# Performance work log

Measured on AMD Instinct MI355X. Metric: run time of the kernel, lower is better.

The kernel has to match this reference:

```python
import jax, jax.numpy as jnp
import numpy as np

N = 120000   # nodes
E = 1200000  # edges
F_IN = 14    # PascalVOC-SP node features
H = 64       # args.hidden
C = 21       # num_classes
EPS = 1e-5


def _glorot(k, shape):
    fan_in = shape[0]
    return jax.random.normal(k, shape, jnp.float32) / np.sqrt(fan_in).astype(np.float32)


def setup_inputs() -> dict:
    key = jax.random.key(0)
    ks = jax.random.split(key, 16)
    inp = {}
    inp['x1'] = jax.random.normal(ks[0], (N, F_IN), jnp.float32)
    inp['edge_index'] = jax.random.randint(ks[1], (2, E), 0, N)
    dims = [(F_IN, H), (H, H), (H, H), (H, H)]
    i = 2
    for l, (din, dout) in enumerate(dims, 1):
        inp[f'Wn{l}'] = _glorot(ks[i], (din, dout)); i += 1
        inp[f'Wr{l}'] = _glorot(ks[i], (din, dout)); i += 1
        inp[f'b{l}'] = jnp.zeros((dout,), jnp.float32)
    for l in (1, 2, 3):
        inp[f'g{l}'] = jnp.ones((H,), jnp.float32)
        inp[f'be{l}'] = jnp.zeros((H,), jnp.float32)
    inp['Wm0'] = _glorot(ks[10], (H, H))
    inp['gm0'] = jnp.ones((H,), jnp.float32)
    inp['bem0'] = jnp.zeros((H,), jnp.float32)
    inp['Wm1'] = _glorot(ks[11], (H, H))
    inp['gm1'] = jnp.ones((H,), jnp.float32)
    inp['bem1'] = jnp.zeros((H,), jnp.float32)
    inp['Wm2'] = _glorot(ks[12], (H, C))
    inp['bm2'] = jnp.zeros((C,), jnp.float32)
    return inp


def _bn(x, g, b):
    # BatchNorm1d forward with batch statistics (train-mode normalization, biased var)
    m = x.mean(axis=0)
    v = x.var(axis=0)
    return (x - m) * jax.lax.rsqrt(v + EPS) * g + b


def _sage(x, src, dst, Wn, Wr, b):
    # PyG SAGEConv (mean aggr): out = mean_neighbors @ Wn + b + x @ Wr
    s = jax.ops.segment_sum(x[src], dst, num_segments=N)        # [N, d]
    cnt = jax.ops.segment_sum(jnp.ones((src.shape[0],), x.dtype), dst, num_segments=N)
    mean = s / jnp.maximum(cnt, 1.0)[:, None]
    return mean @ Wn + b + x @ Wr


def _lrelu(z):
    return jnp.where(z > 0, z, 0.01 * z)


def reference(x1, edge_index, Wn1, Wr1, b1, Wn2, Wr2, b2, Wn3, Wr3, b3, Wn4, Wr4, b4,
              g1, be1, g2, be2, g3, be3, Wm0, gm0, bem0, Wm1, gm1, bem1, Wm2, bm2):
    src, dst = edge_index[0], edge_index[1]
    x = _bn(_lrelu(_sage(x1, src, dst, Wn1, Wr1, b1)), g1, be1)   # conv1 + bano1 (dropout off)
    x = _bn(_lrelu(_sage(x, src, dst, Wn2, Wr2, b2)), g2, be2)    # conv2 + bano2
    x = _bn(jax.nn.relu(_sage(x, src, dst, Wn3, Wr3, b3)), g3, be3)  # conv3 + bano3
    x = _sage(x, src, dst, Wn4, Wr4, b4)                          # conv4
    # mlpRep: Linear(no bias)->BN->ReLU x2, then Linear(bias), no final act
    x = jax.nn.relu(_bn(x @ Wm0, gm0, bem0))
    x = jax.nn.relu(_bn(x @ Wm1, gm1, bem1))
    return x @ Wm2 + bm2
```

## Files before the change

kernel.cpp:

```cpp
#include <hip/hip_runtime.h>

constexpr int NN = 120000;
constexpr int EE = 1200000;
constexpr float EPSV = 1e-5f;
constexpr int NCBLK   = (NN + 127) / 128;
constexpr int NMFMABLK = NN / 64;
constexpr int ASTRIDE = 32;
constexpr int NSLOT = 64;

constexpr int BNODES  = 128;
constexpr int NBUCK   = (NN + BNODES - 1) / BNODES;
constexpr int BSTRIDE = 1536;
constexpr int EPB3    = 8192;
constexpr int NB3     = (EE + EPB3 - 1) / EPB3;

typedef __attribute__((ext_vector_type(8))) short bf8v;
typedef __attribute__((ext_vector_type(4))) float f4v;

__device__ __forceinline__ float bf2f(unsigned short u){
  union { unsigned i; float f; } v; v.i = ((unsigned)u) << 16; return v.f;
}
__device__ __forceinline__ unsigned short f2bf(float f){
  union { float f; unsigned i; } v; v.f = f;
  unsigned u = v.i;
  return (unsigned short)((u + 0x7FFFu + ((u >> 16) & 1u)) >> 16);
}
__device__ __forceinline__ unsigned pack2(float a, float b){
  return (unsigned)f2bf(a) | ((unsigned)f2bf(b) << 16);
}
__device__ __forceinline__ float act_f(float z, int ACT){
  if (ACT == 1) return z > 0.0f ? z : 0.01f*z;
  if (ACT == 2) return fmaxf(z, 0.0f);
  return z;
}
__device__ __forceinline__ void acc8(uint4 u, float& a0, float& a1, float& a2, float& a3,
                                     float& a4, float& a5, float& a6, float& a7){
  a0 += bf2f((unsigned short)(u.x & 0xFFFF)); a1 += bf2f((unsigned short)(u.x >> 16));
  a2 += bf2f((unsigned short)(u.y & 0xFFFF)); a3 += bf2f((unsigned short)(u.y >> 16));
  a4 += bf2f((unsigned short)(u.z & 0xFFFF)); a5 += bf2f((unsigned short)(u.z >> 16));
  a6 += bf2f((unsigned short)(u.w & 0xFFFF)); a7 += bf2f((unsigned short)(u.w >> 16));
}

__global__ __launch_bounds__(512) void k_bucket(const int* __restrict__ src, const int* __restrict__ dst,
                                                int* __restrict__ cursor, unsigned* __restrict__ bucketed){
  __shared__ int hist[NBUCK];
  __shared__ int lstart[NBUCK];
  const int tid = threadIdx.x;
  const int e0  = blockIdx.x * EPB3;
  for (int i = tid; i < NBUCK; i += 512) hist[i] = 0;
  __syncthreads();

  const bool full = (e0 + EPB3 <= EE);
  if (full){
    #pragma unroll 4
    for (int k = 0; k < EPB3/512; k++){
      int d = dst[e0 + k*512 + tid];
      atomicAdd(&hist[d >> 7], 1);
    }
  } else {
    #pragma unroll 1
    for (int k = 0; k < EPB3/512; k++){
      int e = e0 + k*512 + tid;
      if (e < EE){
        int d = dst[e];
        atomicAdd(&hist[d >> 7], 1);
      }
    }
  }
  __syncthreads();
  for (int i = tid; i < NBUCK; i += 512){
    int h = hist[i];
    lstart[i] = (h > 0) ? atomicAdd(&cursor[i], h) : 0;
  }
  __syncthreads();
  for (int i = tid; i < NBUCK; i += 512) hist[i] = 0;
  __syncthreads();
  #pragma unroll 1
  for (int k = 0; k < EPB3/512; k++){
    int e = e0 + k*512 + tid;
    if (e < EE){
      int d = dst[e];
      int s = src[e];
      int b = d >> 7;
      int r = atomicAdd(&hist[b], 1);
      int idx = lstart[b] + r;
      if (idx < BSTRIDE)
        bucketed[(size_t)b*BSTRIDE + idx] = ((unsigned)s << 7) | (unsigned)(d & 127);
    }
  }
}

__global__ __launch_bounds__(256) void k_buildadj(const unsigned* __restrict__ bucketed,
                                                  const int* __restrict__ cursor,
                                                  int* __restrict__ cnt, int* __restrict__ adj,
                                                  float* __restrict__ invdeg){
  __shared__ alignas(16) int ladj[BNODES*ASTRIDE];
  __shared__ int lcnt[BNODES];
  const int tid = threadIdx.x;
  const int b   = blockIdx.x;
  if (tid < BNODES) lcnt[tid] = 0;
  __syncthreads();
  const int tot = min(cursor[b], BSTRIDE);
  const unsigned* rp = bucketed + (size_t)b*BSTRIDE;
  for (int e = tid; e < tot; e += 256){
    unsigned rec = rp[e];
    int d = (int)(rec & 127u);
    int s = (int)(rec >> 7);
    int p = atomicAdd(&lcnt[d], 1);
    if (p < ASTRIDE) ladj[d*ASTRIDE + p] = s;
  }
  __syncthreads();
  int4* ap = (int4*)(adj + (size_t)b*BNODES*ASTRIDE);
  const int4* lp = (const int4*)ladj;
  #pragma unroll
  for (int i = 0; i < (BNODES*ASTRIDE/4)/256; i++)
    ap[i*256 + tid] = lp[i*256 + tid];
  if (tid < BNODES){
    int c = lcnt[tid];
    int n = b*BNODES + tid;
    cnt[n] = c;
    invdeg[n] = (c > 0) ? (1.0f/(float)c) : -1.0f;
  }
}

__global__ __launch_bounds__(256) void k_gather14(const float* __restrict__ x,
                                                  const int* __restrict__ cnt, const int* __restrict__ adj,
                                                  float* __restrict__ agg){
  const int lane = threadIdx.x & 63;
  const int f = lane & 15, g = lane >> 4;
  const int wave = blockIdx.x*4 + (threadIdx.x >> 6);
  const int nwav = gridDim.x*4;
  for (int n = wave; n < NN; n += nwav){
    int d = min(cnt[n], ASTRIDE);
    const int st = n*ASTRIDE;
    float acc = 0.0f;
    for (int j = g; j < d; j += 4){
      int s = adj[st+j];
      if (f < 14) acc += x[(size_t)s*14 + f];
    }
    acc += __shfl_down(acc, 32);
    acc += __shfl_down(acc, 16);
    if (lane < 14) agg[(size_t)n*14 + lane] = acc;
  }
}

__global__ __launch_bounds__(256) void k_prep(const float* __restrict__ Wn, const float* __restrict__ Wr,
                                              const float* __restrict__ b,
                                              float* __restrict__ wbuf, int din){
  int t = threadIdx.x;
  for (int i = t; i < din*64; i += 256){
    wbuf[i]          = Wn[i];
    wbuf[din*64 + i] = Wr[i];
  }
  if (t < 64){
    wbuf[2*din*64 + t]      = b ? b[t] : 0.0f;
    wbuf[2*din*64 + 64 + t] = 0.0f;
  }
}

__global__ __launch_bounds__(256) void k_prep_conv_frag(const float* __restrict__ Wn, const float* __restrict__ Wr,
                                                        const float* __restrict__ b, const float* __restrict__ statSlots,
                                                        const float* __restrict__ g, const float* __restrict__ be,
                                                        unsigned short* __restrict__ frag, float* __restrict__ bias2){
  __shared__ float sc[64], sh[64];
  int t = threadIdx.x;
  if (t < 64){
    float sum = 0.0f, sq = 0.0f;
    #pragma unroll 8
    for (int s = 0; s < NSLOT; s++){
      sum += statSlots[s*128 + t];
      sq  += statSlots[s*128 + 64 + t];
    }
    float m = sum * (1.0f/NN);
    float v = sq * (1.0f/NN) - m*m;
    float a = g[t] * rsqrtf(v + EPSV);
    sc[t] = a; sh[t] = be[t] - m*a;
  }
  __syncthreads();
  if (blockIdx.x == 0 && t < 64){
    float accB = b[t], accN = 0.0f;
    for (int k=0;k<64;k++){
      accB += sh[k]*Wr[k*64+t];
      accN += sh[k]*Wn[k*64+t];
    }
    bias2[t]      = accB;
    bias2[64 + t] = accN;
  }
  {
    int idx = blockIdx.x*256 + t;
    int j    = idx & 7;
    int lane = (idx >> 3) & 63;
    int kk   = (idx >> 9) & 1;
    int ct   = (idx >> 10) & 3;
    int mat  = (idx >> 12) & 1;
    int k    = kk*32 + (lane >> 4)*8 + j;
    int col  = ct*16 + (lane & 15);
    const float* W = mat ? Wr : Wn;
    frag[idx] = f2bf(sc[k] * W[k*64 + col]);
  }
}

__global__ __launch_bounds__(256) void k_prep_lin_frag(const float* __restrict__ W,
                                                       unsigned short* __restrict__ frag,
                                                       float* __restrict__ bias2,
                                                       const float* __restrict__ bnSlots,
                                                       float* __restrict__ bnRed){
  int t = threadIdx.x;
  if (blockIdx.x == 0 && t < 128){
    bias2[t] = 0.0f;
    if (bnSlots){
      float s = 0.0f;
      #pragma unroll 8
      for (int sl = 0; sl < NSLOT; sl++) s += bnSlots[sl*128 + t];
      bnRed[t] = s;
    }
  }
  {
    int idx = blockIdx.x*256 + t;
    int j    = idx & 7;
    int lane = (idx >> 3) & 63;
    int kk   = (idx >> 9) & 1;
    int ct   = (idx >> 10) & 3;
    int k    = kk*32 + (lane >> 4)*8 + j;
    int col  = ct*16 + (lane & 15);
    frag[idx] = f2bf(W[k*64 + col]);
  }
}

template<int ACT, bool STATS>
__global__ __launch_bounds__(256, 1) void k_gmfma(const unsigned short* __restrict__ X,
                                                  const int* __restrict__ cnt, const int* __restrict__ adj,
                                                  const float* __restrict__ invdeg,
                                                  const unsigned short* __restrict__ frag,
                                                  const float* __restrict__ bias2,
                                                  unsigned short* __restrict__ out,
                                                  float* __restrict__ statsOut){
  __shared__ unsigned short sMean[64*72];
  __shared__ float sst[512];
  const int tid  = threadIdx.x;
  const int lane = tid & 63;
  const int wv   = tid >> 6;
  const int nb0  = blockIdx.x*64;

  {
    const int q8 = lane & 7;
    const int h8 = lane >> 3;
    #pragma unroll
    for (int t8 = 0; t8 < 2; t8++){
      const int row = wv*16 + h8*2 + t8;
      const int n   = nb0 + row;
      const int d   = min(cnt[n], ASTRIDE);
      const int st  = n*ASTRIDE;
      float a0=0,a1=0,a2=0,a3=0,a4=0,a5=0,a6=0,a7=0;
      int j = 0;
      for (; j + 7 < d; j += 8){
        int4 sa = *(const int4*)(adj + st + j);
        int4 sb = *(const int4*)(adj + st + j + 4);
        uint4 u0 = *(const uint4*)(X + (size_t)sa.x*64 + 8*q8);
        uint4 u1 = *(const uint4*)(X + (size_t)sa.y*64 + 8*q8);
        uint4 u2 = *(const uint4*)(X + (size_t)sa.z*64 + 8*q8);
        uint4 u3 = *(const uint4*)(X + (size_t)sa.w*64 + 8*q8);
        uint4 u4 = *(const uint4*)(X + (size_t)sb.x*64 + 8*q8);
        uint4 u5 = *(const uint4*)(X + (size_t)sb.y*64 + 8*q8);
        uint4 u6 = *(const uint4*)(X + (size_t)sb.z*64 + 8*q8);
        uint4 u7 = *(const uint4*)(X + (size_t)sb.w*64 + 8*q8);
        acc8(u0,a0,a1,a2,a3,a4,a5,a6,a7); acc8(u1,a0,a1,a2,a3,a4,a5,a6,a7);
        acc8(u2,a0,a1,a2,a3,a4,a5,a6,a7); acc8(u3,a0,a1,a2,a3,a4,a5,a6,a7);
        acc8(u4,a0,a1,a2,a3,a4,a5,a6,a7); acc8(u5,a0,a1,a2,a3,a4,a5,a6,a7);
        acc8(u6,a0,a1,a2,a3,a4,a5,a6,a7); acc8(u7,a0,a1,a2,a3,a4,a5,a6,a7);
      }
      for (; j + 3 < d; j += 4){
        int4 sa = *(const int4*)(adj + st + j);
        uint4 u0 = *(const uint4*)(X + (size_t)sa.x*64 + 8*q8);
        uint4 u1 = *(const uint4*)(X + (size_t)sa.y*64 + 8*q8);
        uint4 u2 = *(const uint4*)(X + (size_t)sa.z*64 + 8*q8);
        uint4 u3 = *(const uint4*)(X + (size_t)sa.w*64 + 8*q8);
        acc8(u0,a0,a1,a2,a3,a4,a5,a6,a7); acc8(u1,a0,a1,a2,a3,a4,a5,a6,a7);
        acc8(u2,a0,a1,a2,a3,a4,a5,a6,a7); acc8(u3,a0,a1,a2,a3,a4,a5,a6,a7);
      }
      for (; j < d; j++){
        int s = adj[st + j];
        uint4 u = *(const uint4*)(X + (size_t)s*64 + 8*q8);
        acc8(u,a0,a1,a2,a3,a4,a5,a6,a7);
      }
      float iv = fmaxf(invdeg[n], 0.0f);
      uint4 o;
      o.x = pack2(a0*iv, a1*iv);
      o.y = pack2(a2*iv, a3*iv);
      o.z = pack2(a4*iv, a5*iv);
      o.w = pack2(a6*iv, a7*iv);
      *(uint4*)(sMean + row*72 + 8*q8) = o;
    }
  }

  const bf8v* fp = (const bf8v*)frag;
  bf8v wn[4][2], wr[4][2];
  #pragma unroll
  for (int ct=0;ct<4;ct++){
    #pragma unroll
    for (int kk=0;kk<2;kk++){
      wn[ct][kk] = fp[((0*4+ct)*2+kk)*64 + lane];
      wr[ct][kk] = fp[((1*4+ct)*2+kk)*64 + lane];
    }
  }
  const int m  = lane & 15;
  const int kq = lane >> 4;
  const size_t arow = (size_t)(nb0 + wv*16 + m)*64;
  bf8v ax0 = *(const bf8v*)(X + arow + kq*8);
  bf8v ax1 = *(const bf8v*)(X + arow + 32 + kq*8);
  __syncthreads();
  bf8v am0 = *(const bf8v*)(sMean + (wv*16 + m)*72 + kq*8);
  bf8v am1 = *(const bf8v*)(sMean + (wv*16 + m)*72 + 32 + kq*8);

  f4v acc[4];
  #pragma unroll
  for (int ct=0;ct<4;ct++){
    f4v c = {0.0f,0.0f,0.0f,0.0f};
    c = __builtin_amdgcn_mfma_f32_16x16x32_bf16(am0, wn[ct][0], c, 0,0,0);
    c = __builtin_amdgcn_mfma_f32_16x16x32_bf16(am1, wn[ct][1], c, 0,0,0);
    c = __builtin_amdgcn_mfma_f32_16x16x32_bf16(ax0, wr[ct][0], c, 0,0,0);
    c = __builtin_amdgcn_mfma_f32_16x16x32_bf16(ax1, wr[ct][1], c, 0,0,0);
    acc[ct] = c;
  }

  const int col = lane & 15;
  float bb[4], bg[4];
  #pragma unroll
  for (int ct=0;ct<4;ct++){
    bb[ct] = bias2[ct*16 + col];
    bg[ct] = bias2[64 + ct*16 + col];
  }
  float ls[4] = {0,0,0,0}, lq[4] = {0,0,0,0};
  #pragma unroll
  for (int r=0;r<4;r++){
    const int node = nb0 + wv*16 + (lane>>4)*4 + r;
    float gadd = (invdeg[node] > 0.0f) ? 1.0f : 0.0f;
    #pragma unroll
    for (int ct=0;ct<4;ct++){
      float z = acc[ct][r] + bb[ct] + gadd * bg[ct];
      z = act_f(z, ACT);
      out[(size_t)node*64 + ct*16 + col] = f2bf(z);
      if (STATS){ ls[ct] += z; lq[ct] = fmaf(z, z, lq[ct]); }
    }
  }
  if constexpr (STATS){
    #pragma unroll
    for (int ct=0;ct<4;ct++){
      float s = ls[ct]; s += __shfl_down(s, 32); s += __shfl_down(s, 16);
      float q = lq[ct]; q += __shfl_down(q, 32); q += __shfl_down(q, 16);
      if (kq == 0){
        sst[wv*128 + ct*16 + col]      = s;
        sst[wv*128 + 64 + ct*16 + col] = q;
      }
    }
    __syncthreads();
    if (tid < 128){
      float v = sst[tid] + sst[128+tid] + sst[256+tid] + sst[384+tid];
      atomicAdd(&statsOut[(blockIdx.x & (NSLOT-1))*128 + tid], v);
    }
  }
}

template<int ACT, bool STATS, bool BNA>
__global__ __launch_bounds__(256, 1) void k_mfma_lin(const unsigned short* __restrict__ Ax,
                                                     const unsigned short* __restrict__ frag,
                                                     const float* __restrict__ bias2,
                                                     unsigned short* __restrict__ out,
                                                     float* __restrict__ statsOut,
                                                     const float* __restrict__ bnRed,
                                                     const float* __restrict__ bnG,
                                                     const float* __restrict__ bnB){
  __shared__ float sst[512];
  const int lane = threadIdx.x & 63;
  const int wv   = threadIdx.x >> 6;
  const int n0   = (blockIdx.x*4 + wv)*16;
  const int m    = lane & 15;
  const int kq   = lane >> 4;

  const bf8v* fp = (const bf8v*)frag;
  bf8v wr[4][2];
  #pragma unroll
  for (int ct=0;ct<4;ct++){
    #pragma unroll
    for (int kk=0;kk<2;kk++) wr[ct][kk] = fp[(ct*2+kk)*64 + lane];
  }

  const size_t arow = (size_t)(n0 + m)*64;
  bf8v ax0 = *(const bf8v*)(Ax + arow + kq*8);
  bf8v ax1 = *(const bf8v*)(Ax + arow + 32 + kq*8);
  if constexpr (BNA){
    #pragma unroll
    for (int j=0;j<8;j++){
      int k0 = kq*8 + j, k1 = 32 + kq*8 + j;
      float m0 = bnRed[k0]*(1.0f/NN);
      float v0 = bnRed[64+k0]*(1.0f/NN) - m0*m0;
      float a0 = bnG[k0]*rsqrtf(v0+EPSV);
      float b0 = bnB[k0] - m0*a0;
      ax0[j] = (short)f2bf(fmaxf(fmaf(a0, bf2f((unsigned short)ax0[j]), b0), 0.0f));
      float m1 = bnRed[k1]*(1.0f/NN);
      float v1 = bnRed[64+k1]*(1.0f/NN) - m1*m1;
      float a1 = bnG[k1]*rsqrtf(v1+EPSV);
      float b1 = bnB[k1] - m1*a1;
      ax1[j] = (short)f2bf(fmaxf(fmaf(a1, bf2f((unsigned short)ax1[j]), b1), 0.0f));
    }
  }

  f4v acc[4];
  #pragma unroll
  for (int ct=0;ct<4;ct++){
    f4v c = {0.0f,0.0f,0.0f,0.0f};
    c = __builtin_amdgcn_mfma_f32_16x16x32_bf16(ax0, wr[ct][0], c, 0,0,0);
    c = __builtin_amdgcn_mfma_f32_16x16x32_bf16(ax1, wr[ct][1], c, 0,0,0);
    acc[ct] = c;
  }

  const int col = lane & 15;
  float bb[4];
  #pragma unroll
  for (int ct=0;ct<4;ct++) bb[ct] = bias2[ct*16 + col];
  float ls[4] = {0,0,0,0}, lq[4] = {0,0,0,0};
  #pragma unroll
  for (int r=0;r<4;r++){
    const int node = n0 + (lane>>4)*4 + r;
    #pragma unroll
    for (int ct=0;ct<4;ct++){
      float z = act_f(acc[ct][r] + bb[ct], ACT);
      out[(size_t)node*64 + ct*16 + col] = f2bf(z);
      if (STATS){ ls[ct] += z; lq[ct] = fmaf(z, z, lq[ct]); }
    }
  }
  if constexpr (STATS){
    #pragma unroll
    for (int ct=0;ct<4;ct++){
      float s = ls[ct]; s += __shfl_down(s, 32); s += __shfl_down(s, 16);
      float q = lq[ct]; q += __shfl_down(q, 32); q += __shfl_down(q, 16);
      if (kq == 0){
        sst[wv*128 + ct*16 + col]      = s;
        sst[wv*128 + 64 + ct*16 + col] = q;
      }
    }
    __syncthreads();
    if (threadIdx.x < 128){
      float v = sst[threadIdx.x] + sst[128+threadIdx.x] + sst[256+threadIdx.x] + sst[384+threadIdx.x];
      atomicAdd(&statsOut[(blockIdx.x & (NSLOT-1))*128 + threadIdx.x], v);
    }
  }
}

__global__ __launch_bounds__(128, 1) void k_gemm_conv14(const float* __restrict__ agg, const float* __restrict__ x,
                                                        const float* __restrict__ invdeg, const float* __restrict__ wbuf,
                                                        unsigned short* __restrict__ out, float* __restrict__ statsOut){
  constexpr int DIN = 14, RS = 15;
  __shared__ float sRow[128*RS];
  const int tid = threadIdx.x;
  const int lane = tid & 63;
  const int n0  = blockIdx.x*128;
  const int n   = n0 + tid;

  {
    const float* gp = agg + (size_t)n0*DIN;
    for (int i = tid; i < 128*DIN; i += 128){
      int r = i / DIN, c = i - r*DIN;
      sRow[r*RS + c] = (n0 + r < NN) ? gp[i] : 0.0f;
    }
  }
  __syncthreads();

  float accA0[32], accA1[32];
  #pragma unroll
  for (int jj=0;jj<32;jj++){ accA0[jj]=0.0f; accA1[jj]=0.0f; }

  #pragma unroll 1
  for (int k=0;k<DIN;k++){
    float rv = sRow[tid*RS + k];
    const float* wr = wbuf + k*64;
    #pragma unroll
    for (int jj=0;jj<32;jj++) accA0[jj] = fmaf(wr[jj],    rv, accA0[jj]);
    #pragma unroll
    for (int jj=0;jj<32;jj++) accA1[jj] = fmaf(wr[32+jj], rv, accA1[jj]);
  }
  __syncthreads();
  {
    const float* gp = x + (size_t)n0*DIN;
    for (int i = tid; i < 128*DIN; i += 128){
      int r = i / DIN, c = i - r*DIN;
      sRow[r*RS + c] = (n0 + r < NN) ? gp[i] : 0.0f;
    }
  }
  __syncthreads();

  const bool valid = (n < NN);
  float iv = valid ? invdeg[n] : -1.0f;
  const bool gate = iv > 0.0f;
  const float* bagg = wbuf + 2*DIN*64 + 64;
  #pragma unroll
  for (int jj=0;jj<32;jj++){
    accA0[jj] = gate ? fmaf(accA0[jj], iv, bagg[jj])    : 0.0f;
    accA1[jj] = gate ? fmaf(accA1[jj], iv, bagg[32+jj]) : 0.0f;
  }

  #pragma unroll 1
  for (int k=0;k<DIN;k++){
    float rv = sRow[tid*RS + k];
    const float* wr = wbuf + DIN*64 + k*64;
    #pragma unroll
    for (int jj=0;jj<32;jj++) accA0[jj] = fmaf(wr[jj],    rv, accA0[jj]);
    #pragma unroll
    for (int jj=0;jj<32;jj++) accA1[jj] = fmaf(wr[32+jj], rv, accA1[jj]);
  }

  const float* bb = wbuf + 2*DIN*64;
  uint2* o2 = (uint2*)(out + (size_t)n*64);
  float vs[64], vq[64];
  #pragma unroll
  for (int q=0;q<8;q++){
    float z0 = valid ? act_f(accA0[4*q+0]+bb[4*q+0],1) : 0.0f;
    float z1 = valid ? act_f(accA0[4*q+1]+bb[4*q+1],1) : 0.0f;
    float z2 = valid ? act_f(accA0[4*q+2]+bb[4*q+2],1) : 0.0f;
    float z3 = valid ? act_f(accA0[4*q+3]+bb[4*q+3],1) : 0.0f;
    vs[4*q+0] = z0; vs[4*q+1] = z1; vs[4*q+2] = z2; vs[4*q+3] = z3;
    if (valid){ uint2 t; t.x = pack2(z0,z1); t.y = pack2(z2,z3); o2[q] = t; }
  }
  #pragma unroll
  for (int q=0;q<8;q++){
    float z0 = valid ? act_f(accA1[4*q+0]+bb[32+4*q+0],1) : 0.0f;
    float z1 = valid ? act_f(accA1[4*q+1]+bb[32+4*q+1],1) : 0.0f;
    float z2 = valid ? act_f(accA1[4*q+2]+bb[32+4*q+2],1) : 0.0f;
    float z3 = valid ? act_f(accA1[4*q+3]+bb[32+4*q+3],1) : 0.0f;
    vs[32+4*q+0] = z0; vs[32+4*q+1] = z1; vs[32+4*q+2] = z2; vs[32+4*q+3] = z3;
    if (valid){ uint2 t; t.x = pack2(z0,z1); t.y = pack2(z2,z3); o2[8+q] = t; }
  }
  #pragma unroll
  for (int j=0;j<64;j++) vq[j] = vs[j]*vs[j];

  #pragma unroll
  for (int k=0;k<6;k++){
    const bool keep1 = ((lane >> k) & 1) != 0;
    const int half = 64 >> (k+1);
    #pragma unroll
    for (int i=0;i<half;i++){
      float sa = vs[2*i], sb = vs[2*i+1];
      float qa = vq[2*i], qb = vq[2*i+1];
      float skeep = keep1 ? sb : sa;
      float ssend = keep1 ? sa : sb;
      float qkeep = keep1 ? qb : qa;
      float qsend = keep1 ? qa : qb;
      vs[i] = skeep + __shfl_xor(ssend, 1<<k);
      vq[i] = qkeep + __shfl_xor(qsend, 1<<k);
    }
  }
  const int slot = (blockIdx.x & (NSLOT-1))*128;
  atomicAdd(&statsOut[slot + lane],      vs[0]);
  atomicAdd(&statsOut[slot + 64 + lane], vq[0]);
}

__global__ __launch_bounds__(256, 1) void k_lin21(const unsigned short* __restrict__ x,
                                                  const float* __restrict__ W, const float* __restrict__ bias,
                                                  const float* __restrict__ st5,
                                                  const float* __restrict__ g5, const float* __restrict__ be5,
                                                  float* __restrict__ out){
  __shared__ float sW[64*21];
  __shared__ float sRed[128];
  __shared__ float sAff[128];
  const int tid = threadIdx.x;
  if (tid < 128){
    float s = 0.0f;
    #pragma unroll 8
    for (int sl = 0; sl < NSLOT; sl++) s += st5[sl*128 + tid];
    sRed[tid] = s;
  }
  for (int i = tid; i < 64*21; i += 256) sW[i] = W[i];
  __syncthreads();
  if (tid < 64){
    float m = sRed[tid]*(1.0f/NN);
    float v = sRed[64+tid]*(1.0f/NN) - m*m;
    float a = g5[tid]*rsqrtf(v+EPSV);
    sAff[tid]    = a;
    sAff[64+tid] = be5[tid] - m*a;
  }
  __syncthreads();

  const int p  = tid & 3;
  const int nl = tid >> 2;
  const int n  = blockIdx.x*64 + nl;
  const bool valid = (n < NN);
  const int k0 = p*16;

  uint4 u0 = {0,0,0,0}, u1 = {0,0,0,0};
  if (valid){
    const unsigned short* rp = x + (size_t)n*64 + k0;
    u0 = *(const uint4*)(rp);
    u1 = *(const uint4*)(rp + 8);
  }
  float f[16];
  f[0]=bf2f((unsigned short)(u0.x&0xFFFF)); f[1]=bf2f((unsigned short)(u0.x>>16));
  f[2]=bf2f((unsigned short)(u0.y&0xFFFF)); f[3]=bf2f((unsigned short)(u0.y>>16));
  f[4]=bf2f((unsigned short)(u0.z&0xFFFF)); f[5]=bf2f((unsigned short)(u0.z>>16));
  f[6]=bf2f((unsigned short)(u0.w&0xFFFF)); f[7]=bf2f((unsigned short)(u0.w>>16));
  f[8]=bf2f((unsigned short)(u1.x&0xFFFF)); f[9]=bf2f((unsigned short)(u1.x>>16));
  f[10]=bf2f((unsigned short)(u1.y&0xFFFF)); f[11]=bf2f((unsigned short)(u1.y>>16));
  f[12]=bf2f((unsigned short)(u1.z&0xFFFF)); f[13]=bf2f((unsigned short)(u1.z>>16));
  f[14]=bf2f((unsigned short)(u1.w&0xFFFF)); f[15]=bf2f((unsigned short)(u1.w>>16));
  #pragma unroll
  for (int j=0;j<16;j++)
    f[j] = fmaxf(fmaf(sAff[k0+j], f[j], sAff[64+k0+j]), 0.0f);

  float a[21];
  #pragma unroll
  for (int jj=0;jj<21;jj++) a[jj] = 0.0f;
  #pragma unroll
  for (int k=0;k<16;k++){
    const float* wr = sW + (k0+k)*21;
    float rv = f[k];
    #pragma unroll
    for (int jj=0;jj<21;jj++) a[jj] = fmaf(wr[jj], rv, a[jj]);
  }
  #pragma unroll
  for (int jj=0;jj<21;jj++){
    a[jj] += __shfl_xor(a[jj], 1);
    a[jj] += __shfl_xor(a[jj], 2);
  }
  if (valid){
    const int c0 = p*6;
    const int ce = (p == 3) ? 21 : c0 + 6;
    float* op = out + (size_t)n*21;
    #pragma unroll 6
    for (int jj=c0; jj<ce; jj++) op[jj] = a[jj] + bias[jj];
  }
}

extern "C" void kernel_launch(void* const* d_in, const int* in_sizes, int n_in,
                              void* d_out, int out_size, void* d_ws, size_t ws_size,
                              hipStream_t stream){
  const float* x1  = (const float*)d_in[0];
  const int*   ei  = (const int*)d_in[1];
  const int* srcp = ei;
  const int* dstp = ei + EE;
  const float *Wn1=(const float*)d_in[2],  *Wr1=(const float*)d_in[3],  *b1=(const float*)d_in[4];
  const float *Wn2=(const float*)d_in[5],  *Wr2=(const float*)d_in[6],  *b2=(const float*)d_in[7];
  const float *Wn3=(const float*)d_in[8],  *Wr3=(const float*)d_in[9],  *b3=(const float*)d_in[10];
  const float *Wn4=(const float*)d_in[11], *Wr4=(const float*)d_in[12], *b4=(const float*)d_in[13];
  const float *g1=(const float*)d_in[14], *be1=(const float*)d_in[15];
  const float *g2=(const float*)d_in[16], *be2=(const float*)d_in[17];
  const float *g3=(const float*)d_in[18], *be3=(const float*)d_in[19];
  const float *Wm0=(const float*)d_in[20], *gm0=(const float*)d_in[21], *bem0=(const float*)d_in[22];
  const float *Wm1=(const float*)d_in[23], *gm1=(const float*)d_in[24], *bem1=(const float*)d_in[25];
  const float *Wm2=(const float*)d_in[26], *bm2=(const float*)d_in[27];
  float* out = (float*)d_out;

  char* ws = (char*)d_ws;
  int*   cnt     = (int*)(ws);
  float* invdeg  = (float*)(ws + (1ull<<20));
  int*   adj     = (int*)(ws + (2ull<<20));
  float* agg14   = (float*)(ws + (18ull<<20));
  unsigned short* hA   = (unsigned short*)(ws + (25ull<<20));
  unsigned short* hB   = (unsigned short*)(ws + (41ull<<20));
  float* stats   = (float*)(ws + (57ull<<20));
  float* bnRed   = (float*)(ws + (57ull<<20) + 192*1024);
  float* wbuf    = (float*)(ws + (57ull<<20) + 256*1024);
  unsigned short* fragC = (unsigned short*)(ws + (58ull<<20));
  float* bias2C  = (float*)(ws + (58ull<<20) + 65536);
  unsigned short* fragL = (unsigned short*)(ws + (59ull<<20));
  float* bias2L  = (float*)(ws + (59ull<<20) + 65536);
  unsigned* bucketed = (unsigned*)(ws + (25ull<<20));
  int* cursor        = (int*)(ws + (25ull<<20) + (6ull<<20));

  float* S1 = stats;
  float* S2 = stats + NSLOT*128;
  float* S3 = stats + 2*NSLOT*128;
  float* S4 = stats + 3*NSLOT*128;
  float* S5 = stats + 4*NSLOT*128;

  hipMemsetAsync(cursor, 0, NBUCK*sizeof(int), stream);
  hipMemsetAsync(stats, 0, 5*NSLOT*128*sizeof(float), stream);
  k_bucket  <<<NB3,  512,0,stream>>>(srcp, dstp, cursor, bucketed);
  k_buildadj<<<NBUCK,256,0,stream>>>(bucketed, cursor, cnt, adj, invdeg);

  k_gather14<<<2048,256,0,stream>>>(x1, cnt, adj, agg14);
  k_prep<<<1,256,0,stream>>>(Wn1,Wr1,b1,wbuf,14);
  k_gemm_conv14<<<NCBLK,128,0,stream>>>(agg14,x1,invdeg,wbuf,hA,S1);

  k_prep_conv_frag<<<32,256,0,stream>>>(Wn2,Wr2,b2,S1,g1,be1,fragC,bias2C);
  k_gmfma<1,true><<<NMFMABLK,256,0,stream>>>(hA,cnt,adj,invdeg,fragC,bias2C,hB,S2);

  k_prep_conv_frag<<<32,256,0,stream>>>(Wn3,Wr3,b3,S2,g2,be2,fragC,bias2C);
  k_gmfma<2,true><<<NMFMABLK,256,0,stream>>>(hB,cnt,adj,invdeg,fragC,bias2C,hA,S3);

  k_prep_conv_frag<<<32,256,0,stream>>>(Wn4,Wr4,b4,S3,g3,be3,fragC,bias2C);
  k_gmfma<0,false><<<NMFMABLK,256,0,stream>>>(hA,cnt,adj,invdeg,fragC,bias2C,hB,nullptr);

  k_prep_lin_frag<<<16,256,0,stream>>>(Wm0, fragL, bias2L, nullptr, nullptr);
  k_mfma_lin<0,true,false><<<NMFMABLK,256,0,stream>>>(hB,fragL,bias2L,hA,S4,nullptr,nullptr,nullptr);

  k_prep_lin_frag<<<16,256,0,stream>>>(Wm1, fragL, bias2L, S4, bnRed);
  k_mfma_lin<0,true,true><<<NMFMABLK,256,0,stream>>>(hA,fragL,bias2L,hB,S5,bnRed,gm0,bem0);

  k_lin21<<<NMFMABLK,256,0,stream>>>(hB,Wm2,bm2,S5,gm1,bem1,out);
}
```

Before: 404.9 us.

## Fold stats memset into bucket kernel, drop weight prep, precompute final BN affine

Zeroing of the BN stats buffer moves into the k_bucket kernel, replacing a separate memset. The k_prep weight-copy kernel is removed, and conv14 now reads Wn/Wr/b directly (the zero aggregate-bias add is dropped). The final BN affine reduction moves out of every k_lin21 block into a single tiny kernel. EPB3 is halved to give k_bucket more blocks. The net launch count barely changes; the gains are from removing redundant per-block slot reduction and small memset/prep overheads, at the cost of a finer bucket pass with more global cursor atomics.

Result: no change. 398.3 us (-1.6%).

```diff
diff --git a/kernel.cpp b/kernel.cpp
--- a/kernel.cpp
+++ b/kernel.cpp
@@ -11,8 +11,9 @@
 constexpr int BNODES  = 128;
 constexpr int NBUCK   = (NN + BNODES - 1) / BNODES;
 constexpr int BSTRIDE = 1536;
-constexpr int EPB3    = 8192;
+constexpr int EPB3    = 4096;
 constexpr int NB3     = (EE + EPB3 - 1) / EPB3;
+constexpr int NSTATF  = 5*NSLOT*128;
 
 typedef __attribute__((ext_vector_type(8))) short bf8v;
 typedef __attribute__((ext_vector_type(4))) float f4v;
@@ -42,11 +43,13 @@
 }
 
 __global__ __launch_bounds__(512) void k_bucket(const int* __restrict__ src, const int* __restrict__ dst,
-                                                int* __restrict__ cursor, unsigned* __restrict__ bucketed){
+                                                int* __restrict__ cursor, unsigned* __restrict__ bucketed,
+                                                float* __restrict__ stats){
   __shared__ int hist[NBUCK];
   __shared__ int lstart[NBUCK];
   const int tid = threadIdx.x;
   const int e0  = blockIdx.x * EPB3;
+  for (int i = blockIdx.x*512 + tid; i < NSTATF; i += NB3*512) stats[i] = 0.0f;
   for (int i = tid; i < NBUCK; i += 512) hist[i] = 0;
   __syncthreads();
 
@@ -144,20 +147,6 @@
   }
 }
 
-__global__ __launch_bounds__(256) void k_prep(const float* __restrict__ Wn, const float* __restrict__ Wr,
-                                              const float* __restrict__ b,
-                                              float* __restrict__ wbuf, int din){
-  int t = threadIdx.x;
-  for (int i = t; i < din*64; i += 256){
-    wbuf[i]          = Wn[i];
-    wbuf[din*64 + i] = Wr[i];
-  }
-  if (t < 64){
-    wbuf[2*din*64 + t]      = b ? b[t] : 0.0f;
-    wbuf[2*din*64 + 64 + t] = 0.0f;
-  }
-}
-
 __global__ __launch_bounds__(256) void k_prep_conv_frag(const float* __restrict__ Wn, const float* __restrict__ Wr,
                                                         const float* __restrict__ b, const float* __restrict__ statSlots,
                                                         const float* __restrict__ g, const float* __restrict__ be,
@@ -225,6 +214,23 @@
     int col  = ct*16 + (lane & 15);
     frag[idx] = f2bf(W[k*64 + col]);
   }
+}
+
+__global__ __launch_bounds__(64) void k_prep_aff(const float* __restrict__ st,
+                                                 const float* __restrict__ g, const float* __restrict__ be,
+                                                 float* __restrict__ aff){
+  int t = threadIdx.x;
+  float s = 0.0f, q = 0.0f;
+  #pragma unroll 8
+  for (int sl = 0; sl < NSLOT; sl++){
+    s += st[sl*128 + t];
+    q += st[sl*128 + 64 + t];
+  }
+  float m = s*(1.0f/NN);
+  float v = q*(1.0f/NN) - m*m;
+  float a = g[t]*rsqrtf(v+EPSV);
+  aff[t]      = a;
+  aff[64 + t] = be[t] - m*a;
 }
 
 template<int ACT, bool STATS>
@@ -448,7 +454,9 @@
 }
 
 __global__ __launch_bounds__(128, 1) void k_gemm_conv14(const float* __restrict__ agg, const float* __restrict__ x,
-                                                        const float* __restrict__ invdeg, const float* __restrict__ wbuf,
+                                                        const float* __restrict__ invdeg,
+                                                        const float* __restrict__ Wn, const float* __restrict__ Wr,
+                                                        const float* __restrict__ b,
                                                         unsigned short* __restrict__ out, float* __restrict__ statsOut){
   constexpr int DIN = 14, RS = 15;
   __shared__ float sRow[128*RS];
@@ -473,7 +481,7 @@
   #pragma unroll 1
   for (int k=0;k<DIN;k++){
     float rv = sRow[tid*RS + k];
-    const float* wr = wbuf + k*64;
+    const float* wr = Wn + k*64;
     #pragma unroll
     for (int jj=0;jj<32;jj++) accA0[jj] = fmaf(wr[jj],    rv, accA0[jj]);
     #pragma unroll
@@ -492,41 +500,39 @@
   const bool valid = (n < NN);
   float iv = valid ? invdeg[n] : -1.0f;
   const bool gate = iv > 0.0f;
-  const float* bagg = wbuf + 2*DIN*64 + 64;
   #pragma unroll
   for (int jj=0;jj<32;jj++){
-    accA0[jj] = gate ? fmaf(accA0[jj], iv, bagg[jj])    : 0.0f;
-    accA1[jj] = gate ? fmaf(accA1[jj], iv, bagg[32+jj]) : 0.0f;
+    accA0[jj] = gate ? accA0[jj]*iv : 0.0f;
+    accA1[jj] = gate ? accA1[jj]*iv : 0.0f;
   }
 
   #pragma unroll 1
   for (int k=0;k<DIN;k++){
     float rv = sRow[tid*RS + k];
-    const float* wr = wbuf + DIN*64 + k*64;
+    const float* wr = Wr + k*64;
     #pragma unroll
     for (int jj=0;jj<32;jj++) accA0[jj] = fmaf(wr[jj],    rv, accA0[jj]);
     #pragma unroll
     for (int jj=0;jj<32;jj++) accA1[jj] = fmaf(wr[32+jj], rv, accA1[jj]);
   }
 
-  const float* bb = wbuf + 2*DIN*64;
   uint2* o2 = (uint2*)(out + (size_t)n*64);
   float vs[64], vq[64];
   #pragma unroll
   for (int q=0;q<8;q++){
-    float z0 = valid ? act_f(accA0[4*q+0]+bb[4*q+0],1) : 0.0f;
-    float z1 = valid ? act_f(accA0[4*q+1]+bb[4*q+1],1) : 0.0f;
-    float z2 = valid ? act_f(accA0[4*q+2]+bb[4*q+2],1) : 0.0f;
-    float z3 = valid ? act_f(accA0[4*q+3]+bb[4*q+3],1) : 0.0f;
+    float z0 = valid ? act_f(accA0[4*q+0]+b[4*q+0],1) : 0.0f;
+    float z1 = valid ? act_f(accA0[4*q+1]+b[4*q+1],1) : 0.0f;
+    float z2 = valid ? act_f(accA0[4*q+2]+b[4*q+2],1) : 0.0f;
+    float z3 = valid ? act_f(accA0[4*q+3]+b[4*q+3],1) : 0.0f;
     vs[4*q+0] = z0; vs[4*q+1] = z1; vs[4*q+2] = z2; vs[4*q+3] = z3;
     if (valid){ uint2 t; t.x = pack2(z0,z1); t.y = pack2(z2,z3); o2[q] = t; }
   }
   #pragma unroll
   for (int q=0;q<8;q++){
-    float z0 = valid ? act_f(accA1[4*q+0]+bb[32+4*q+0],1) : 0.0f;
-    float z1 = valid ? act_f(accA1[4*q+1]+bb[32+4*q+1],1) : 0.0f;
-    float z2 = valid ? act_f(accA1[4*q+2]+bb[32+4*q+2],1) : 0.0f;
-    float z3 = valid ? act_f(accA1[4*q+3]+bb[32+4*q+3],1) : 0.0f;
+    float z0 = valid ? act_f(accA1[4*q+0]+b[32+4*q+0],1) : 0.0f;
+    float z1 = valid ? act_f(accA1[4*q+1]+b[32+4*q+1],1) : 0.0f;
+    float z2 = valid ? act_f(accA1[4*q+2]+b[32+4*q+2],1) : 0.0f;
+    float z3 = valid ? act_f(accA1[4*q+3]+b[32+4*q+3],1) : 0.0f;
     vs[32+4*q+0] = z0; vs[32+4*q+1] = z1; vs[32+4*q+2] = z2; vs[32+4*q+3] = z3;
     if (valid){ uint2 t; t.x = pack2(z0,z1); t.y = pack2(z2,z3); o2[8+q] = t; }
   }
@@ -556,28 +562,13 @@
 
 __global__ __launch_bounds__(256, 1) void k_lin21(const unsigned short* __restrict__ x,
                                                   const float* __restrict__ W, const float* __restrict__ bias,
-                                                  const float* __restrict__ st5,
-                                                  const float* __restrict__ g5, const float* __restrict__ be5,
+                                                  const float* __restrict__ aff,
                                                   float* __restrict__ out){
   __shared__ float sW[64*21];
-  __shared__ float sRed[128];
   __shared__ float sAff[128];
   const int tid = threadIdx.x;
-  if (tid < 128){
-    float s = 0.0f;
-    #pragma unroll 8
-    for (int sl = 0; sl < NSLOT; sl++) s += st5[sl*128 + tid];
-    sRed[tid] = s;
-  }
+  if (tid < 128) sAff[tid] = aff[tid];
   for (int i = tid; i < 64*21; i += 256) sW[i] = W[i];
-  __syncthreads();
-  if (tid < 64){
-    float m = sRed[tid]*(1.0f/NN);
-    float v = sRed[64+tid]*(1.0f/NN) - m*m;
-    float a = g5[tid]*rsqrtf(v+EPSV);
-    sAff[tid]    = a;
-    sAff[64+tid] = be5[tid] - m*a;
-  }
   __syncthreads();
 
   const int p  = tid & 3;
@@ -657,7 +648,7 @@
   unsigned short* hB   = (unsigned short*)(ws + (41ull<<20));
   float* stats   = (float*)(ws + (57ull<<20));
   float* bnRed   = (float*)(ws + (57ull<<20) + 192*1024);
-  float* wbuf    = (float*)(ws + (57ull<<20) + 256*1024);
+  float* aff5    = (float*)(ws + (57ull<<20) + 224*1024);
   unsigned short* fragC = (unsigned short*)(ws + (58ull<<20));
   float* bias2C  = (float*)(ws + (58ull<<20) + 65536);
   unsigned short* fragL = (unsigned short*)(ws + (59ull<<20));
@@ -672,13 +663,11 @@
   float* S5 = stats + 4*NSLOT*128;
 
   hipMemsetAsync(cursor, 0, NBUCK*sizeof(int), stream);
-  hipMemsetAsync(stats, 0, 5*NSLOT*128*sizeof(float), stream);
-  k_bucket  <<<NB3,  512,0,stream>>>(srcp, dstp, cursor, bucketed);
+  k_bucket  <<<NB3,  512,0,stream>>>(srcp, dstp, cursor, bucketed, stats);
   k_buildadj<<<NBUCK,256,0,stream>>>(bucketed, cursor, cnt, adj, invdeg);
 
   k_gather14<<<2048,256,0,stream>>>(x1, cnt, adj, agg14);
-  k_prep<<<1,256,0,stream>>>(Wn1,Wr1,b1,wbuf,14);
-  k_gemm_conv14<<<NCBLK,128,0,stream>>>(agg14,x1,invdeg,wbuf,hA,S1);
+  k_gemm_conv14<<<NCBLK,128,0,stream>>>(agg14,x1,invdeg,Wn1,Wr1,b1,hA,S1);
 
   k_prep_conv_frag<<<32,256,0,stream>>>(Wn2,Wr2,b2,S1,g1,be1,fragC,bias2C);
   k_gmfma<1,true><<<NMFMABLK,256,0,stream>>>(hA,cnt,adj,invdeg,fragC,bias2C,hB,S2);
@@ -695,5 +684,6 @@
   k_prep_lin_frag<<<16,256,0,stream>>>(Wm1, fragL, bias2L, S4, bnRed);
   k_mfma_lin<0,true,true><<<NMFMABLK,256,0,stream>>>(hA,fragL,bias2L,hB,S5,bnRed,gm0,bem0);
 
-  k_lin21<<<NMFMABLK,256,0,stream>>>(hB,Wm2,bm2,S5,gm1,bem1,out);
-}
+  k_prep_aff<<<1,64,0,stream>>>(S5, gm1, bem1, aff5);
+  k_lin21<<<NMFMABLK,256,0,stream>>>(hB,Wm2,bm2,aff5,out);
+}
```
